# Optimization experiments

Measured on AMD Instinct MI355X. Metric: run time of the kernel, lower is better.

The kernel has to match this reference:

```python
import jax, jax.numpy as jnp
import numpy as np

NUM_HEADS = 12
EPS = 1e-12  # F.normalize default eps


def setup_inputs() -> dict:
    key = jax.random.key(0)
    ks = jax.random.split(key, 6)
    B, N, C, M = 32, 1024, 768, 64
    s = 1.0 / np.sqrt(C)
    return {
        "x": jax.random.normal(ks[0], (B, N, C), jnp.float32),
        "Wc": jax.random.normal(ks[1], (M, C), jnp.float32) * s,
        "bc": jnp.zeros((M,), jnp.float32),
        "Wq": jax.random.normal(ks[2], (C, C), jnp.float32) * s,
        "bq": jnp.zeros((C,), jnp.float32),
        "Wk": jax.random.normal(ks[3], (C, C), jnp.float32) * s,
        "bk": jnp.zeros((C,), jnp.float32),
        "Wv": jax.random.normal(ks[4], (C, C), jnp.float32) * s,
        "bv": jnp.zeros((C,), jnp.float32),
        "Wp": jax.random.normal(ks[5], (C, C), jnp.float32) * s,
        "bp": jnp.zeros((C,), jnp.float32),
    }


def reference(x, Wc, bc, Wq, bq, Wk, bk, Wv, bv, Wp, bp):
    B, N, C = x.shape
    H = NUM_HEADS
    D = C // H
    scale = D ** -0.5

    # Cluster: linear -> transpose -> sigmoid/N -> einsum -> L2 norm
    c = jnp.einsum('bnc,mc->bmn', x, Wc) + bc[None, :, None]   # (B, M, N)
    c = jax.nn.sigmoid(c) / N
    z = jnp.einsum('bmn,bnc->bmc', c, x)                        # (B, M, C)
    z = z / jnp.maximum(jnp.linalg.norm(z, axis=-1, keepdims=True), EPS)

    M = z.shape[1]
    q = (x @ Wq.T + bq).reshape(B, N, H, D).transpose(0, 2, 1, 3)  # (B,H,N,D)
    k = (z @ Wk.T + bk).reshape(B, M, H, D).transpose(0, 2, 1, 3)  # (B,H,M,D)
    v = (z @ Wv.T + bv).reshape(B, M, H, D).transpose(0, 2, 1, 3)  # (B,H,M,D)

    attn = jax.nn.softmax(jnp.einsum('bhnd,bhmd->bhnm', q, k) * scale, axis=-1)
    o = jnp.einsum('bhnm,bhmd->bhnd', attn, v)                  # (B,H,N,D)
    o = o.transpose(0, 2, 1, 3).reshape(B, N, C)
    return o @ Wp.T + bp
```

## Files before the change

### kernel.cpp

```cpp
#include <hip/hip_runtime.h>
#include <hip/hip_bf16.h>
#include <cstdint>

#define BB 32
#define NN 1024
#define CC 768
#define MM 64
#define HH 12
#define DD 64

typedef float f4v __attribute__((ext_vector_type(4)));
typedef __bf16 bf8 __attribute__((ext_vector_type(8)));
typedef __bf16 bf4 __attribute__((ext_vector_type(4)));

__device__ __forceinline__ f4v mfma16(bf8 a, bf8 b, f4v c) {
    return __builtin_amdgcn_mfma_f32_16x16x32_bf16(a, b, c, 0, 0, 0);
}
__device__ __forceinline__ __bf16 f2bf(float f) { return (__bf16)f; }

__device__ __forceinline__ void gl2lds16(const void* g, void* lds) {
    __builtin_amdgcn_global_load_lds((const __attribute__((address_space(1))) void*)g,
                                     (__attribute__((address_space(3))) void*)lds, 16, 0, 0);
}


__global__ __launch_bounds__(256) void k_cvtW(
        const float* __restrict__ Wc, const float* __restrict__ Wq,
        const float* __restrict__ Wk, const float* __restrict__ Wv,
        const float* __restrict__ Wp,
        __bf16* __restrict__ wc, __bf16* __restrict__ wq,
        __bf16* __restrict__ wk, __bf16* __restrict__ wv,
        __bf16* __restrict__ wp) {
    const float* in; __bf16* out; int n4; int frag;
    switch (blockIdx.y) {
        case 0: in = Wc; out = wc; n4 = MM * CC / 4; frag = 1; break;
        case 1: in = Wq; out = wq; n4 = CC * CC / 4; frag = 1; break;
        case 2: in = Wk; out = wk; n4 = CC * CC / 4; frag = 0; break;
        case 3: in = Wv; out = wv; n4 = CC * CC / 4; frag = 0; break;
        default: in = Wp; out = wp; n4 = CC * CC / 4; frag = 1; break;
    }
    int i = blockIdx.x * 256 + threadIdx.x;
    if (i < n4) {
        float4 v = *(const float4*)&in[i * 4];
        bf4 o; o[0] = f2bf(v.x); o[1] = f2bf(v.y); o[2] = f2bf(v.z); o[3] = f2bf(v.w);
        if (frag) {
            int lin = i * 4, m = lin / CC, c = lin % CC;
            size_t off = ((size_t)((m >> 4) * 24 + (c >> 5))) * 512
                       + ((((c >> 3) & 3) * 16) + (m & 15)) * 8 + (c & 7);
            *(bf4*)&out[off] = o;
        } else {
            *(bf4*)&out[i * 4] = o;
        }
    }
}

__global__ __launch_bounds__(256) void k_cvtx(const float* __restrict__ x,
        __bf16* __restrict__ xb, __bf16* __restrict__ xt) {
    int c0 = blockIdx.x * 64, n0 = blockIdx.y * 64, b = blockIdx.z;
    __shared__ __align__(16) __bf16 tileT[64 * 66];
    __shared__ __align__(16) __bf16 tileR[64 * 72];
    int t = threadIdx.x;
#pragma unroll
    for (int i = 0; i < 4; i++) {
        int idx = t + 256 * i, r = idx >> 4, cq = idx & 15;
        float4 v = *(const float4*)&x[((size_t)(b * NN + n0 + r)) * CC + c0 + cq * 4];
        float vv[4] = {v.x, v.y, v.z, v.w};
        bf4 o;
#pragma unroll
        for (int j = 0; j < 4; j++) {
            __bf16 bv = f2bf(vv[j]);
            o[j] = bv;
            tileT[(cq * 4 + j) * 66 + r] = bv;
        }
        *(bf4*)&tileR[r * 72 + cq * 4] = o;
    }
    __syncthreads();
    int gnt = b * 64 + (n0 >> 4);
    int kc0 = c0 >> 5;
    int lane = t & 63;
#pragma unroll
    for (int i = 0; i < 2; i++) {
        int idx = t + 256 * i;
        int nt_loc = idx >> 7, kc_loc = (idx >> 6) & 1;
        int row = nt_loc * 16 + (lane & 15);
        int col = kc_loc * 32 + (lane >> 4) * 8;
        bf8 v = *(const bf8*)&tileR[row * 72 + col];
        *(bf8*)&xb[((size_t)((gnt + nt_loc) * 24 + kc0 + kc_loc)) * 512 + lane * 8] = v;
    }
#pragma unroll
    for (int i = 0; i < 2; i++) {
        int idx = t + 256 * i, c = idx >> 3, ch = idx & 7;
        bf8 v2 = *(const bf8*)&tileT[c * 66 + ch * 8];
        *(bf8*)&xt[((size_t)(b * CC + c0 + c)) * NN + n0 + ch * 8] = v2;
    }
}

__global__ __launch_bounds__(256) void k_cluster(const __bf16* __restrict__ xb,
        const __bf16* __restrict__ Wc, const float* __restrict__ bc,
        __bf16* __restrict__ cbmn) {
    int n0 = blockIdx.x * 128, b = blockIdx.y;
    int t = threadIdx.x, w = t >> 6, l = t & 63, quad = (l >> 4), l16 = l & 15;
    int nt0 = b * 64 + (n0 >> 4);
    f4v acc[2][4];
#pragma unroll
    for (int i = 0; i < 2; i++) for (int j = 0; j < 4; j++) acc[i][j] = (f4v)0.0f;
    for (int kc = 0; kc < 24; kc++) {
        bf8 afr[2], bfr[4];
#pragma unroll
        for (int sr = 0; sr < 2; sr++)
            afr[sr] = *(const bf8*)&xb[((size_t)((nt0 + w * 2 + sr) * 24 + kc)) * 512 + l * 8];
#pragma unroll
        for (int sc = 0; sc < 4; sc++)
            bfr[sc] = *(const bf8*)&Wc[((size_t)(sc * 24 + kc)) * 512 + l * 8];
#pragma unroll
        for (int sr = 0; sr < 2; sr++)
#pragma unroll
            for (int sc = 0; sc < 4; sc++)
                acc[sr][sc] = mfma16(afr[sr], bfr[sc], acc[sr][sc]);
    }
#pragma unroll
    for (int sr = 0; sr < 2; sr++)
#pragma unroll
        for (int sc = 0; sc < 4; sc++) {
            int m = sc * 16 + l16;
            float bias = bc[m];
            bf4 p;
#pragma unroll
            for (int r = 0; r < 4; r++) {
                float val = acc[sr][sc][r] + bias;
                val = 1.0f / (1.0f + __expf(-val));
                p[r] = f2bf(val * (1.0f / 1024.0f));
            }
            *(bf4*)&cbmn[((size_t)(b * MM + m)) * NN + n0 + w * 32 + sr * 16 + quad * 4] = p;
        }
}

__global__ __launch_bounds__(256) void k_z(const __bf16* __restrict__ cbmn,
        const __bf16* __restrict__ xt, float* __restrict__ z) {
    int c0 = blockIdx.x * 64, b = blockIdx.y;
    int t = threadIdx.x, w = t >> 6, l = t & 63, quad = l >> 4, l16 = l & 15;
    f4v acc[4];
#pragma unroll
    for (int j = 0; j < 4; j++) acc[j] = (f4v)0.0f;
    for (int n0 = 0; n0 < NN; n0 += 32) {
        bf8 afr = *(const bf8*)&cbmn[((size_t)(b * MM + w * 16 + l16)) * NN + n0 + quad * 8];
#pragma unroll
        for (int sc = 0; sc < 4; sc++) {
            bf8 bfr = *(const bf8*)&xt[((size_t)(b * CC + c0 + sc * 16 + l16)) * NN + n0 + quad * 8];
            acc[sc] = mfma16(afr, bfr, acc[sc]);
        }
    }
#pragma unroll
    for (int sc = 0; sc < 4; sc++) {
        int cc = c0 + sc * 16 + l16;
#pragma unroll
        for (int r = 0; r < 4; r++) {
            int m = w * 16 + quad * 4 + r;
            z[((size_t)(b * MM + m)) * CC + cc] = acc[sc][r];
        }
    }
}

__global__ __launch_bounds__(256) void k_znorm(const float* __restrict__ z, __bf16* __restrict__ zb) {
    int w = threadIdx.x >> 6, l = threadIdx.x & 63;
    int row = blockIdx.x * 4 + w;
    const float* zr = &z[(size_t)row * CC];
    float v[12]; float ss = 0.f;
#pragma unroll
    for (int i = 0; i < 12; i++) { v[i] = zr[l + i * 64]; ss += v[i] * v[i]; }
#pragma unroll
    for (int off = 32; off; off >>= 1) ss += __shfl_xor(ss, off);
    float s = 1.0f / fmaxf(sqrtf(ss), 1e-12f);
    __bf16* zo = &zb[(size_t)row * CC];
#pragma unroll
    for (int i = 0; i < 12; i++) zo[l + i * 64] = f2bf(v[i] * s);
}

__global__ __launch_bounds__(256) void k_kv(const __bf16* __restrict__ zb,
        const __bf16* __restrict__ Wk, const float* __restrict__ bk,
        const __bf16* __restrict__ Wv, const float* __restrict__ bv,
        __bf16* __restrict__ kout, __bf16* __restrict__ vtout) {
    int ct = blockIdx.x, b = blockIdx.y, which = blockIdx.z;
    const __bf16* W = which ? Wv : Wk;
    const float* bias = which ? bv : bk;
    int t = threadIdx.x, w = t >> 6, l = t & 63, quad = l >> 4, l16 = l & 15;
    f4v acc[4][2];
#pragma unroll
    for (int i = 0; i < 4; i++) for (int j = 0; j < 2; j++) acc[i][j] = (f4v)0.0f;
    for (int k0 = 0; k0 < CC; k0 += 32) {
        bf8 afr[4], bfr[2];
#pragma unroll
        for (int sr = 0; sr < 4; sr++)
            afr[sr] = *(const bf8*)&zb[((size_t)(b * MM + sr * 16 + l16)) * CC + k0 + quad * 8];
#pragma unroll
        for (int sc = 0; sc < 2; sc++)
            bfr[sc] = *(const bf8*)&W[((size_t)(ct * 128 + w * 32 + sc * 16 + l16)) * CC + k0 + quad * 8];
#pragma unroll
        for (int sr = 0; sr < 4; sr++)
#pragma unroll
            for (int sc = 0; sc < 2; sc++)
                acc[sr][sc] = mfma16(afr[sr], bfr[sc], acc[sr][sc]);
    }
#pragma unroll
    for (int sr = 0; sr < 4; sr++)
#pragma unroll
        for (int sc = 0; sc < 2; sc++) {
            int col = ct * 128 + w * 32 + sc * 16 + l16;
            float bb = bias[col];
            int h = col >> 6, d = col & 63;
            if (which == 0) {
#pragma unroll
                for (int r = 0; r < 4; r++) {
                    int m = sr * 16 + quad * 4 + r;
                    kout[(((size_t)(b * HH + h)) * MM + m) * DD + d] = f2bf(acc[sr][sc][r] + bb);
                }
            } else {
                bf4 p;
#pragma unroll
                for (int r = 0; r < 4; r++) p[r] = f2bf(acc[sr][sc][r] + bb);
                *(bf4*)&vtout[(((size_t)(b * HH + h)) * DD + d) * MM + sr * 16 + quad * 4] = p;
            }
        }
}

#define STAGE_AF(Asrc, buf, kcs)                                                      \
    do {                                                                              \
        __bf16* _d = (buf);                                                           \
        gl2lds16(&(Asrc)[((size_t)((gt0 + w) * 24 + (kcs))) * 512 + l * 8], &_d[w * 512]); \
        gl2lds16(&(Asrc)[((size_t)((gt0 + w + 4) * 24 + (kcs))) * 512 + l * 8], &_d[(w + 4) * 512]); \
    } while (0)

#define GEMM_KLOOP_H(Asrc, Bsrc)                                                      \
    bf8 bcur[4], bnxt[4];                                                             \
    _Pragma("unroll")                                                                 \
    for (int sc = 0; sc < 4; sc++)                                                    \
        bcur[sc] = *(const bf8*)&(Bsrc)[((size_t)((jt * 16 + w * 4 + sc) * 24)) * 512 + l * 8]; \
    STAGE_AF(Asrc, As3, 0);                                                           \
    STAGE_AF(Asrc, As3 + 4096, 1);                                                    \
    asm volatile("s_waitcnt vmcnt(2)" ::: "memory");                                  \
    __builtin_amdgcn_s_barrier();                                                     \
    for (int kt = 0; kt < 24; ++kt) {                                                 \
        const __bf16* As = As3 + (kt % 3) * 4096;                                     \
        if (kt < 23) {                                                                \
            _Pragma("unroll")                                                         \
            for (int sc = 0; sc < 4; sc++)                                            \
                bnxt[sc] = *(const bf8*)&(Bsrc)[((size_t)((jt * 16 + w * 4 + sc) * 24 + kt + 1)) * 512 + l * 8]; \
        }                                                                             \
        bf8 afr[8];                                                                   \
        _Pragma("unroll")                                                             \
        for (int sr = 0; sr < 8; sr++)                                                \
            afr[sr] = *(const bf8*)&As[sr * 512 + l * 8];                             \
        __builtin_amdgcn_sched_barrier(0);                                            \
        if (kt < 22) STAGE_AF(Asrc, As3 + ((kt + 2) % 3) * 4096, kt + 2);             \
        __builtin_amdgcn_s_setprio(1);                                                \
        _Pragma("unroll")                                                             \
        for (int sr = 0; sr < 8; sr++)                                                \
            _Pragma("unroll")                                                         \
            for (int sc = 0; sc < 4; sc++)                                            \
                acc[sr][sc] = mfma16(afr[sr], bcur[sc], acc[sr][sc]);                 \
        __builtin_amdgcn_s_setprio(0);                                                \
        if (kt < 23) {                                                                \
            _Pragma("unroll")                                                         \
            for (int sc = 0; sc < 4; sc++) bcur[sc] = bnxt[sc];                       \
        }                                                                             \
        if (kt < 22)       asm volatile("s_waitcnt vmcnt(6)" ::: "memory");           \
        else if (kt == 22) asm volatile("s_waitcnt vmcnt(4)" ::: "memory");           \
        __builtin_amdgcn_s_barrier();                                                 \
    }

__global__ __launch_bounds__(256, 2) void k_qproj(const __bf16* __restrict__ xb,
        const __bf16* __restrict__ Wq, const float* __restrict__ bq,
        __bf16* __restrict__ qb) {
    int orig = blockIdx.x;
    int lid = (orig & 7) * 96 + (orig >> 3);
    int jt = lid % 3;
    int gt0 = (lid / 3) * 8;

    __shared__ __align__(16) __bf16 As3[3 * 4096];
    __shared__ __align__(16) __bf16 eb[128 * 72];
    int t = threadIdx.x, w = t >> 6, l = t & 63, quad = l >> 4, l16 = l & 15;
    f4v acc[8][4];
#pragma unroll
    for (int i = 0; i < 8; i++) for (int j = 0; j < 4; j++) acc[i][j] = (f4v)0.0f;

    GEMM_KLOOP_H(xb, Wq);

    for (int p = 0; p < 4; ++p) {
        if (w == p) {
#pragma unroll
            for (int sc = 0; sc < 4; sc++) {
                int col = jt * 256 + p * 64 + sc * 16 + l16;
                float bb = bq[col];
#pragma unroll
                for (int sr = 0; sr < 8; sr++)
#pragma unroll
                    for (int r = 0; r < 4; r++)
                        eb[(sr * 16 + quad * 4 + r) * 72 + sc * 16 + l16] = f2bf(acc[sr][sc][r] + bb);
            }
        }
        __syncthreads();
        int h = jt * 4 + p;
#pragma unroll
        for (int i = 0; i < 4; i++) {
            int idx = t + 256 * i, nt = idx >> 7, kcs = (idx >> 6) & 1, lane = idx & 63;
            bf8 v = *(const bf8*)&eb[(nt * 16 + (lane & 15)) * 72 + kcs * 32 + (lane >> 4) * 8];
            *(bf8*)&qb[((size_t)(((gt0 + nt) * 12 + h) * 2 + kcs)) * 512 + lane * 8] = v;
        }
        __syncthreads();
    }
}

#define QS 72
__global__ __launch_bounds__(256) void k_attn(const __bf16* __restrict__ qb,
        const __bf16* __restrict__ kb, const __bf16* __restrict__ vt,
        __bf16* __restrict__ ob) {
    int n0 = blockIdx.x * 128, h = blockIdx.y, b = blockIdx.z;
    __shared__ __align__(16) __bf16 ps[128 * QS];
    int t = threadIdx.x, w = t >> 6, l = t & 63, quad = l >> 4, l16 = l & 15;
    size_t bh = (size_t)(b * HH + h);
    int nt0 = b * 64 + (n0 >> 4);

    f4v sacc[2][4];
#pragma unroll
    for (int i = 0; i < 2; i++) for (int j = 0; j < 4; j++) sacc[i][j] = (f4v)0.0f;
#pragma unroll
    for (int kc = 0; kc < 2; kc++) {
        bf8 afr[2], bfr[4];
#pragma unroll
        for (int sr = 0; sr < 2; sr++)
            afr[sr] = *(const bf8*)&qb[((size_t)(((nt0 + w * 2 + sr) * 12 + h) * 2 + kc)) * 512 + l * 8];
#pragma unroll
        for (int sc = 0; sc < 4; sc++)
            bfr[sc] = *(const bf8*)&kb[(bh * MM + sc * 16 + l16) * DD + kc * 32 + quad * 8];
#pragma unroll
        for (int sr = 0; sr < 2; sr++)
#pragma unroll
            for (int sc = 0; sc < 4; sc++)
                sacc[sr][sc] = mfma16(afr[sr], bfr[sc], sacc[sr][sc]);
    }
#pragma unroll
    for (int sr = 0; sr < 2; sr++) {
#pragma unroll
        for (int r = 0; r < 4; r++) {
            float mx = -1e30f;
#pragma unroll
            for (int sc = 0; sc < 4; sc++) mx = fmaxf(mx, sacc[sr][sc][r] * 0.125f);
#pragma unroll
            for (int off = 1; off < 16; off <<= 1) mx = fmaxf(mx, __shfl_xor(mx, off));
            float e[4]; float sum = 0.f;
#pragma unroll
            for (int sc = 0; sc < 4; sc++) { e[sc] = __expf(sacc[sr][sc][r] * 0.125f - mx); sum += e[sc]; }
#pragma unroll
            for (int off = 1; off < 16; off <<= 1) sum += __shfl_xor(sum, off);
            float inv = 1.0f / sum;
            int row = w * 32 + sr * 16 + quad * 4 + r;
#pragma unroll
            for (int sc = 0; sc < 4; sc++) ps[row * QS + sc * 16 + l16] = f2bf(e[sc] * inv);
        }
    }
    f4v oacc[2][4];
#pragma unroll
    for (int i = 0; i < 2; i++) for (int j = 0; j < 4; j++) oacc[i][j] = (f4v)0.0f;
#pragma unroll
    for (int kc = 0; kc < 2; kc++) {
        bf8 afr[2], bfr[4];
#pragma unroll
        for (int sr = 0; sr < 2; sr++)
            afr[sr] = *(const bf8*)&ps[(w * 32 + sr * 16 + l16) * QS + kc * 32 + quad * 8];
#pragma unroll
        for (int sc = 0; sc < 4; sc++)
            bfr[sc] = *(const bf8*)&vt[(bh * DD + sc * 16 + l16) * MM + kc * 32 + quad * 8];
#pragma unroll
        for (int sr = 0; sr < 2; sr++)
#pragma unroll
            for (int sc = 0; sc < 4; sc++)
                oacc[sr][sc] = mfma16(afr[sr], bfr[sc], oacc[sr][sc]);
    }
#pragma unroll
    for (int sr = 0; sr < 2; sr++)
#pragma unroll
        for (int sc = 0; sc < 4; sc++) {
            int row = w * 32 + sr * 16;
#pragma unroll
            for (int r = 0; r < 4; r++)
                ps[(row + quad * 4 + r) * QS + sc * 16 + l16] = f2bf(oacc[sr][sc][r]);
        }
    __syncthreads();
#pragma unroll
    for (int i = 0; i < 4; i++) {
        int idx = t + 256 * i, nt = idx >> 7, kcs = (idx >> 6) & 1, lane = idx & 63;
        bf8 v = *(const bf8*)&ps[(nt * 16 + (lane & 15)) * QS + kcs * 32 + (lane >> 4) * 8];
        *(bf8*)&ob[((size_t)((nt0 + nt) * 24 + h * 2 + kcs)) * 512 + lane * 8] = v;
    }
}

__global__ __launch_bounds__(256, 2) void k_oproj(const __bf16* __restrict__ ob,
        const __bf16* __restrict__ Wp, const float* __restrict__ bp,
        float* __restrict__ out) {
    int orig = blockIdx.x;
    int lid = (orig & 7) * 96 + (orig >> 3);
    int jt = lid % 3;
    int gt0 = (lid / 3) * 8;
    size_t arow0 = (size_t)(lid / 3) * 128;

    __shared__ __align__(16) __bf16 As3[3 * 4096];
    __shared__ __align__(16) float ebf[128 * 68];
    int t = threadIdx.x, w = t >> 6, l = t & 63, quad = l >> 4, l16 = l & 15;
    f4v acc[8][4];
#pragma unroll
    for (int i = 0; i < 8; i++) for (int j = 0; j < 4; j++) acc[i][j] = (f4v)0.0f;

    GEMM_KLOOP_H(ob, Wp);

    for (int p = 0; p < 4; ++p) {
        if (w == p) {
#pragma unroll
            for (int sc = 0; sc < 4; sc++) {
                int col = jt * 256 + p * 64 + sc * 16 + l16;
                float bb = bp[col];
#pragma unroll
                for (int sr = 0; sr < 8; sr++)
#pragma unroll
                    for (int r = 0; r < 4; r++)
                        ebf[(sr * 16 + quad * 4 + r) * 68 + sc * 16 + l16] = acc[sr][sc][r] + bb;
            }
        }
        __syncthreads();
#pragma unroll
        for (int i = 0; i < 8; i++) {
            int idx = t + 256 * i, row = idx >> 4, c4 = idx & 15;
            *(float4*)&out[(arow0 + row) * CC + jt * 256 + p * 64 + c4 * 4] = *(const float4*)&ebf[row * 68 + c4 * 4];
        }
        __syncthreads();
    }
}

extern "C" void kernel_launch(void* const* d_in, const int* in_sizes, int n_in,
                              void* d_out, int out_size, void* d_ws, size_t ws_size,
                              hipStream_t stream) {
    (void)in_sizes; (void)n_in; (void)out_size; (void)ws_size;
    const float* x  = (const float*)d_in[0];
    const float* Wc = (const float*)d_in[1];
    const float* bc = (const float*)d_in[2];
    const float* Wq = (const float*)d_in[3];
    const float* bq = (const float*)d_in[4];
    const float* Wk = (const float*)d_in[5];
    const float* bk = (const float*)d_in[6];
    const float* Wv = (const float*)d_in[7];
    const float* bv = (const float*)d_in[8];
    const float* Wp = (const float*)d_in[9];
    const float* bp = (const float*)d_in[10];
    float* out = (float*)d_out;

    char* ws = (char*)d_ws;
    size_t off = 0;
    auto alloc = [&](size_t bytes) { void* p = ws + off; off = (off + bytes + 255) & ~(size_t)255; return p; };
    __bf16* wc_b = (__bf16*)alloc((size_t)MM * CC * 2);
    __bf16* wq_b = (__bf16*)alloc((size_t)CC * CC * 2);
    __bf16* wk_b = (__bf16*)alloc((size_t)CC * CC * 2);
    __bf16* wv_b = (__bf16*)alloc((size_t)CC * CC * 2);
    __bf16* wp_b = (__bf16*)alloc((size_t)CC * CC * 2);
    __bf16* xb   = (__bf16*)alloc((size_t)BB * NN * CC * 2);
    __bf16* xt_o = (__bf16*)alloc((size_t)BB * NN * CC * 2);
    __bf16* q_b  = (__bf16*)alloc((size_t)BB * NN * CC * 2);
    __bf16* c_bmn= (__bf16*)alloc((size_t)BB * MM * NN * 2);
    float*  z_f  = (float*) alloc((size_t)BB * MM * CC * 4);
    __bf16* z_b  = (__bf16*)alloc((size_t)BB * MM * CC * 2);
    __bf16* k_b  = (__bf16*)alloc((size_t)BB * HH * MM * DD * 2);
    __bf16* v_t  = (__bf16*)alloc((size_t)BB * HH * MM * DD * 2);

    k_cvtW<<<dim3((CC * CC / 4 + 255) / 256, 5), 256, 0, stream>>>(
        Wc, Wq, Wk, Wv, Wp, wc_b, wq_b, wk_b, wv_b, wp_b);

    k_cvtx<<<dim3(CC / 64, NN / 64, BB), 256, 0, stream>>>(x, xb, xt_o);
    k_cluster<<<dim3(NN / 128, BB), 256, 0, stream>>>(xb, wc_b, bc, c_bmn);
    k_z<<<dim3(CC / 64, BB), 256, 0, stream>>>(c_bmn, xt_o, z_f);
    k_znorm<<<(BB * MM) / 4, 256, 0, stream>>>(z_f, z_b);
    k_kv<<<dim3(CC / 128, BB, 2), 256, 0, stream>>>(z_b, wk_b, bk, wv_b, bv, k_b, v_t);
    k_qproj<<<dim3((BB * NN / 128) * 3), 256, 0, stream>>>(xb, wq_b, bq, q_b);
    k_attn<<<dim3(NN / 128, HH, BB), 256, 0, stream>>>(q_b, k_b, v_t, xt_o );
    k_oproj<<<dim3((BB * NN / 128) * 3), 256, 0, stream>>>(xt_o, wp_b, bp, out);
}
```

Measured before the change: 265.7 us.

## Deepen GEMM K-loop pipeline to two K-steps per barrier and loop cvtx over channels

The q-projection and output-projection GEMM K-loop now processes two 32-wide K chunks per iteration, using a 6-slot LDS ring and double B-register buffers. This halves the number of barriers and keeps more global loads in flight. The epilogue staging buffer now reuses the ring LDS instead of a separate allocation, which offsets the larger ring. Separately, k_cvtx has each block loop over all 12 channel tiles, cutting the grid by 12x. That reduces launch parallelism and adds more barriers per block, and the GEMM change raises register pressure from the extra B fragments.

```diff
diff --git a/kernel.cpp b/kernel.cpp
--- a/kernel.cpp
+++ b/kernel.cpp
@@ -56,42 +56,45 @@
 
 __global__ __launch_bounds__(256) void k_cvtx(const float* __restrict__ x,
         __bf16* __restrict__ xb, __bf16* __restrict__ xt) {
-    int c0 = blockIdx.x * 64, n0 = blockIdx.y * 64, b = blockIdx.z;
+    int n0 = blockIdx.x * 64, b = blockIdx.y;
     __shared__ __align__(16) __bf16 tileT[64 * 66];
     __shared__ __align__(16) __bf16 tileR[64 * 72];
     int t = threadIdx.x;
-#pragma unroll
-    for (int i = 0; i < 4; i++) {
-        int idx = t + 256 * i, r = idx >> 4, cq = idx & 15;
-        float4 v = *(const float4*)&x[((size_t)(b * NN + n0 + r)) * CC + c0 + cq * 4];
-        float vv[4] = {v.x, v.y, v.z, v.w};
-        bf4 o;
-#pragma unroll
-        for (int j = 0; j < 4; j++) {
-            __bf16 bv = f2bf(vv[j]);
-            o[j] = bv;
-            tileT[(cq * 4 + j) * 66 + r] = bv;
-        }
-        *(bf4*)&tileR[r * 72 + cq * 4] = o;
-    }
-    __syncthreads();
     int gnt = b * 64 + (n0 >> 4);
-    int kc0 = c0 >> 5;
     int lane = t & 63;
-#pragma unroll
-    for (int i = 0; i < 2; i++) {
-        int idx = t + 256 * i;
-        int nt_loc = idx >> 7, kc_loc = (idx >> 6) & 1;
-        int row = nt_loc * 16 + (lane & 15);
-        int col = kc_loc * 32 + (lane >> 4) * 8;
-        bf8 v = *(const bf8*)&tileR[row * 72 + col];
-        *(bf8*)&xb[((size_t)((gnt + nt_loc) * 24 + kc0 + kc_loc)) * 512 + lane * 8] = v;
-    }
-#pragma unroll
-    for (int i = 0; i < 2; i++) {
-        int idx = t + 256 * i, c = idx >> 3, ch = idx & 7;
-        bf8 v2 = *(const bf8*)&tileT[c * 66 + ch * 8];
-        *(bf8*)&xt[((size_t)(b * CC + c0 + c)) * NN + n0 + ch * 8] = v2;
+    for (int ci = 0; ci < 12; ci++) {
+        int c0 = ci * 64;
+        if (ci) __syncthreads();
+#pragma unroll
+        for (int i = 0; i < 4; i++) {
+            int idx = t + 256 * i, r = idx >> 4, cq = idx & 15;
+            float4 v = *(const float4*)&x[((size_t)(b * NN + n0 + r)) * CC + c0 + cq * 4];
+            float vv[4] = {v.x, v.y, v.z, v.w};
+            bf4 o;
+#pragma unroll
+            for (int j = 0; j < 4; j++) {
+                __bf16 bv = f2bf(vv[j]);
+                o[j] = bv;
+                tileT[(cq * 4 + j) * 66 + r] = bv;
+            }
+            *(bf4*)&tileR[r * 72 + cq * 4] = o;
+        }
+        __syncthreads();
+#pragma unroll
+        for (int i = 0; i < 2; i++) {
+            int idx = t + 256 * i;
+            int nt_loc = idx >> 7, kc_loc = (idx >> 6) & 1;
+            int row = nt_loc * 16 + (lane & 15);
+            int col = kc_loc * 32 + (lane >> 4) * 8;
+            bf8 v = *(const bf8*)&tileR[row * 72 + col];
+            *(bf8*)&xb[((size_t)((gnt + nt_loc) * 24 + ci * 2 + kc_loc)) * 512 + lane * 8] = v;
+        }
+#pragma unroll
+        for (int i = 0; i < 2; i++) {
+            int idx = t + 256 * i, c = idx >> 3, ch = idx & 7;
+            bf8 v2 = *(const bf8*)&tileT[c * 66 + ch * 8];
+            *(bf8*)&xt[((size_t)(b * CC + c0 + c)) * NN + n0 + ch * 8] = v2;
+        }
     }
 }
 
@@ -230,41 +233,62 @@
         gl2lds16(&(Asrc)[((size_t)((gt0 + w + 4) * 24 + (kcs))) * 512 + l * 8], &_d[(w + 4) * 512]); \
     } while (0)
 
-#define GEMM_KLOOP_H(Asrc, Bsrc)                                                      \
-    bf8 bcur[4], bnxt[4];                                                             \
-    _Pragma("unroll")                                                                 \
-    for (int sc = 0; sc < 4; sc++)                                                    \
-        bcur[sc] = *(const bf8*)&(Bsrc)[((size_t)((jt * 16 + w * 4 + sc) * 24)) * 512 + l * 8]; \
-    STAGE_AF(Asrc, As3, 0);                                                           \
-    STAGE_AF(Asrc, As3 + 4096, 1);                                                    \
-    asm volatile("s_waitcnt vmcnt(2)" ::: "memory");                                  \
+#define BLD(dst, Bsrc, kcs)                                                           \
+    do {                                                                              \
+        _Pragma("unroll")                                                             \
+        for (int _sc = 0; _sc < 4; _sc++)                                             \
+            dst[_sc] = *(const bf8*)&(Bsrc)[((size_t)((jt * 16 + w * 4 + _sc) * 24 + (kcs))) * 512 + l * 8]; \
+    } while (0)
+
+#define GEMM_KLOOP_H2(Asrc, Bsrc)                                                     \
+    bf8 bcur[2][4], bnxt[2][4];                                                       \
+    BLD(bcur[0], Bsrc, 0);                                                            \
+    BLD(bcur[1], Bsrc, 1);                                                            \
+    STAGE_AF(Asrc, As6, 0);                                                           \
+    STAGE_AF(Asrc, As6 + 4096, 1);                                                    \
+    STAGE_AF(Asrc, As6 + 2 * 4096, 2);                                                \
+    STAGE_AF(Asrc, As6 + 3 * 4096, 3);                                                \
+    asm volatile("s_waitcnt vmcnt(4)" ::: "memory");                                  \
     __builtin_amdgcn_s_barrier();                                                     \
-    for (int kt = 0; kt < 24; ++kt) {                                                 \
-        const __bf16* As = As3 + (kt % 3) * 4096;                                     \
-        if (kt < 23) {                                                                \
-            _Pragma("unroll")                                                         \
-            for (int sc = 0; sc < 4; sc++)                                            \
-                bnxt[sc] = *(const bf8*)&(Bsrc)[((size_t)((jt * 16 + w * 4 + sc) * 24 + kt + 1)) * 512 + l * 8]; \
-        }                                                                             \
+    for (int i = 0; i < 12; ++i) {                                                    \
+        if (i < 11) { BLD(bnxt[0], Bsrc, 2 * i + 2); BLD(bnxt[1], Bsrc, 2 * i + 3); } \
+        const __bf16* As0 = As6 + ((2 * i) % 6) * 4096;                               \
+        const __bf16* As1 = As6 + ((2 * i + 1) % 6) * 4096;                           \
         bf8 afr[8];                                                                   \
         _Pragma("unroll")                                                             \
         for (int sr = 0; sr < 8; sr++)                                                \
-            afr[sr] = *(const bf8*)&As[sr * 512 + l * 8];                             \
+            afr[sr] = *(const bf8*)&As0[sr * 512 + l * 8];                            \
         __builtin_amdgcn_sched_barrier(0);                                            \
-        if (kt < 22) STAGE_AF(Asrc, As3 + ((kt + 2) % 3) * 4096, kt + 2);             \
+        if (i < 10) {                                                                 \
+            STAGE_AF(Asrc, As6 + ((2 * i + 4) % 6) * 4096, 2 * i + 4);                \
+            STAGE_AF(Asrc, As6 + ((2 * i + 5) % 6) * 4096, 2 * i + 5);                \
+        }                                                                             \
         __builtin_amdgcn_s_setprio(1);                                                \
         _Pragma("unroll")                                                             \
         for (int sr = 0; sr < 8; sr++)                                                \
             _Pragma("unroll")                                                         \
             for (int sc = 0; sc < 4; sc++)                                            \
-                acc[sr][sc] = mfma16(afr[sr], bcur[sc], acc[sr][sc]);                 \
+                acc[sr][sc] = mfma16(afr[sr], bcur[0][sc], acc[sr][sc]);              \
         __builtin_amdgcn_s_setprio(0);                                                \
-        if (kt < 23) {                                                                \
+        _Pragma("unroll")                                                             \
+        for (int sr = 0; sr < 8; sr++)                                                \
+            afr[sr] = *(const bf8*)&As1[sr * 512 + l * 8];                            \
+        __builtin_amdgcn_sched_barrier(0);                                            \
+        __builtin_amdgcn_s_setprio(1);                                                \
+        _Pragma("unroll")                                                             \
+        for (int sr = 0; sr < 8; sr++)                                                \
             _Pragma("unroll")                                                         \
-            for (int sc = 0; sc < 4; sc++) bcur[sc] = bnxt[sc];                       \
+            for (int sc = 0; sc < 4; sc++)                                            \
+                acc[sr][sc] = mfma16(afr[sr], bcur[1][sc], acc[sr][sc]);              \
+        __builtin_amdgcn_s_setprio(0);                                                \
+        if (i < 11) {                                                                 \
+            _Pragma("unroll")                                                         \
+            for (int h2 = 0; h2 < 2; h2++)                                            \
+                _Pragma("unroll")                                                     \
+                for (int sc = 0; sc < 4; sc++) bcur[h2][sc] = bnxt[h2][sc];           \
         }                                                                             \
-        if (kt < 22)       asm volatile("s_waitcnt vmcnt(6)" ::: "memory");           \
-        else if (kt == 22) asm volatile("s_waitcnt vmcnt(4)" ::: "memory");           \
+        if (i < 10)       asm volatile("s_waitcnt vmcnt(12)" ::: "memory");           \
+        else if (i == 10) asm volatile("s_waitcnt vmcnt(8)" ::: "memory");            \
         __builtin_amdgcn_s_barrier();                                                 \
     }
 
@@ -276,15 +300,15 @@
     int jt = lid % 3;
     int gt0 = (lid / 3) * 8;
 
-    __shared__ __align__(16) __bf16 As3[3 * 4096];
-    __shared__ __align__(16) __bf16 eb[128 * 72];
+    __shared__ __align__(16) __bf16 As6[6 * 4096];
     int t = threadIdx.x, w = t >> 6, l = t & 63, quad = l >> 4, l16 = l & 15;
     f4v acc[8][4];
 #pragma unroll
     for (int i = 0; i < 8; i++) for (int j = 0; j < 4; j++) acc[i][j] = (f4v)0.0f;
 
-    GEMM_KLOOP_H(xb, Wq);
-
+    GEMM_KLOOP_H2(xb, Wq);
+
+    __bf16* eb = As6;
     for (int p = 0; p < 4; ++p) {
         if (w == p) {
 #pragma unroll
@@ -403,15 +427,15 @@
     int gt0 = (lid / 3) * 8;
     size_t arow0 = (size_t)(lid / 3) * 128;
 
-    __shared__ __align__(16) __bf16 As3[3 * 4096];
-    __shared__ __align__(16) float ebf[128 * 68];
+    __shared__ __align__(16) __bf16 As6[6 * 4096];
     int t = threadIdx.x, w = t >> 6, l = t & 63, quad = l >> 4, l16 = l & 15;
     f4v acc[8][4];
 #pragma unroll
     for (int i = 0; i < 8; i++) for (int j = 0; j < 4; j++) acc[i][j] = (f4v)0.0f;
 
-    GEMM_KLOOP_H(ob, Wp);
-
+    GEMM_KLOOP_H2(ob, Wp);
+
+    float* ebf = (float*)As6;
     for (int p = 0; p < 4; ++p) {
         if (w == p) {
 #pragma unroll
@@ -472,7 +496,7 @@
     k_cvtW<<<dim3((CC * CC / 4 + 255) / 256, 5), 256, 0, stream>>>(
         Wc, Wq, Wk, Wv, Wp, wc_b, wq_b, wk_b, wv_b, wp_b);
 
-    k_cvtx<<<dim3(CC / 64, NN / 64, BB), 256, 0, stream>>>(x, xb, xt_o);
+    k_cvtx<<<dim3(NN / 64, BB), 256, 0, stream>>>(x, xb, xt_o);
     k_cluster<<<dim3(NN / 128, BB), 256, 0, stream>>>(xb, wc_b, bc, c_bmn);
     k_z<<<dim3(CC / 64, BB), 256, 0, stream>>>(c_bmn, xt_o, z_f);
     k_znorm<<<(BB * MM) / 4, 256, 0, stream>>>(z_f, z_b);
```

After: 280.1 us. 5.4% more time.
